# Kernel optimization log

Hardware: AMD Instinct MI355X
Metric: run time of the kernel (lower is better)

Reference implementation:

```python
import jax, jax.numpy as jnp
import numpy as np

B, Hres, Wres, DIM = 2, 56, 56, 256
HEADS, K = 8, 7


def setup_inputs() -> dict:
    key = jax.random.key(0)
    ks = jax.random.split(key, 6)
    return {
        "x": jax.random.normal(ks[0], (B, Hres, Wres, DIM), dtype=jnp.float32),
        "q_extra": jax.random.normal(ks[1], (B, Hres, Wres, DIM), dtype=jnp.float32),
        "kv_w": jax.random.normal(ks[2], (2 * DIM, DIM), dtype=jnp.float32) * 0.02,
        "kv_b": jnp.zeros((2 * DIM,), dtype=jnp.float32),
        "rpb": jax.random.normal(ks[3], (HEADS, 2 * K - 1, 2 * K - 1), dtype=jnp.float32) * 0.02,
        "proj_w": jax.random.normal(ks[4], (DIM, DIM), dtype=jnp.float32) * 0.02,
        "proj_b": jnp.zeros((DIM,), dtype=jnp.float32),
    }


def _window_idx(L, k):
    # NATTEN clamped window start: clip(i - k//2, 0, L - k)
    r = k // 2
    start = jnp.clip(jnp.arange(L) - r, 0, L - k)  # [L]
    return start[:, None] + jnp.arange(k)[None, :]  # [L, k]


def _pb_idx(L, k):
    # NATTEN relative-position-bias start index per query position
    r = k // 2
    i = jnp.arange(L)
    pb_start = r + jnp.maximum(r - i, 0) + jnp.minimum(L - i - 1 - r, 0)  # [L]
    return pb_start[:, None] + jnp.arange(k)[None, :]  # [L, k]


def reference(x, q_extra, kv_w, kv_b, rpb, proj_w, proj_b):
    Bn, H, W, C = x.shape
    heads = rpb.shape[0]
    k = (rpb.shape[1] + 1) // 2
    hd = C // heads
    scale = hd ** (-0.5)

    # q: [B, heads, H, W, hd]
    q = q_extra.reshape(Bn, H, W, heads, hd).transpose(0, 3, 1, 2, 4) * scale
    # kv projection -> key, value: [B, heads, H, W, hd]
    kv = (x @ kv_w.T + kv_b).reshape(Bn, H, W, 2, heads, hd).transpose(3, 0, 4, 1, 2, 5)
    key, val = kv[0], kv[1]

    idx_h = _window_idx(H, k)  # [H, k]
    idx_w = _window_idx(W, k)  # [W, k]

    # gather neighborhood windows: [B, heads, H, k, W, k, hd]
    k_win = key[:, :, idx_h][:, :, :, :, idx_w]
    v_win = val[:, :, idx_h][:, :, :, :, idx_w]

    # QK over neighborhood: [B, heads, H, W, k, k]
    attn = jnp.einsum('nhijd,nhiajbd->nhijab', q, k_win)

    # relative positional bias: [heads, H, k, W, k] -> [heads, H, W, k, k]
    pb_i = _pb_idx(H, k)
    pb_j = _pb_idx(W, k)
    bias = rpb[:, pb_i[:, :, None, None], pb_j[None, None, :, :]]
    attn = attn + bias.transpose(0, 1, 3, 2, 4)[None]

    attn = jax.nn.softmax(attn.reshape(Bn, heads, H, W, k * k), axis=-1)
    attn = attn.reshape(Bn, heads, H, W, k, k)

    # AV: [B, heads, H, W, hd]
    out = jnp.einsum('nhijab,nhiajbd->nhijd', attn, v_win)
    out = out.transpose(0, 2, 3, 1, 4).reshape(Bn, H, W, C)
    return out @ proj_w.T + proj_b
```

## Files before the change

kernel.cpp:

```cpp
#include <hip/hip_runtime.h>
#include <hip/hip_bf16.h>

#define BB 2
#define HH 56
#define WW 56
#define CC 256
#define HEADS 8
#define HD 32
#define KW 7
#define NPIX (BB*HH*WW)
#define KV_N 512

using bf16x8 = __attribute__((ext_vector_type(8))) short;
using f32x4  = __attribute__((ext_vector_type(4))) float;

__device__ __forceinline__ ushort f2bf(float f) {
    union { float f; uint u; } v; v.f = f;
    uint r = v.u + 0x7FFF + ((v.u >> 16) & 1);
    return (ushort)(r >> 16);
}
__device__ __forceinline__ float bf2f(ushort h) {
    union { uint u; float f; } v; v.u = ((uint)h) << 16;
    return v.f;
}

template<int BM, int BN, bool A_BF16, bool OUT_BF16>
__global__ __launch_bounds__(256) void gemm_bf16_nt(
    const void* __restrict__ Av, const float* __restrict__ Wt,
    const float* __restrict__ bias, void* __restrict__ Cv,
    int M, int N, int Kd)
{
    constexpr int BK  = 64;
    constexpr int LDT = 72;
    constexpr int WTM = BM / 2, WTN = BN / 2;
    constexpr int MF  = WTM / 16, NF = WTN / 16;

    __shared__ ushort As[BM][LDT];
    __shared__ ushort Bs[BN][LDT];

    const int tid  = threadIdx.x;
    const int lane = tid & 63;
    const int wid  = tid >> 6;
    const int wm   = wid >> 1;
    const int wn   = wid & 1;
    const int bm   = blockIdx.y * BM;
    const int bn   = blockIdx.x * BN;

    const int srow = tid >> 3;
    const int skq  = (tid & 7) * 8;

    f32x4 acc[MF][NF] = {};

    for (int k0 = 0; k0 < Kd; k0 += BK) {
        #pragma unroll
        for (int p = 0; p < BM / 32; ++p) {
            const int r = p * 32 + srow;
            if constexpr (A_BF16) {
                const ushort* src = (const ushort*)Av + (size_t)(bm + r) * Kd + k0 + skq;
                *(bf16x8*)&As[r][skq] = *(const bf16x8*)src;
            } else {
                const float* src = (const float*)Av + (size_t)(bm + r) * Kd + k0 + skq;
                float4 f0 = *(const float4*)(src);
                float4 f1 = *(const float4*)(src + 4);
                bf16x8 v;
                v[0]=f2bf(f0.x); v[1]=f2bf(f0.y); v[2]=f2bf(f0.z); v[3]=f2bf(f0.w);
                v[4]=f2bf(f1.x); v[5]=f2bf(f1.y); v[6]=f2bf(f1.z); v[7]=f2bf(f1.w);
                *(bf16x8*)&As[r][skq] = v;
            }
        }
        #pragma unroll
        for (int p = 0; p < BN / 32; ++p) {
            const int r = p * 32 + srow;
            const float* src = Wt + (size_t)(bn + r) * Kd + k0 + skq;
            float4 f0 = *(const float4*)(src);
            float4 f1 = *(const float4*)(src + 4);
            bf16x8 v;
            v[0]=f2bf(f0.x); v[1]=f2bf(f0.y); v[2]=f2bf(f0.z); v[3]=f2bf(f0.w);
            v[4]=f2bf(f1.x); v[5]=f2bf(f1.y); v[6]=f2bf(f1.z); v[7]=f2bf(f1.w);
            *(bf16x8*)&Bs[r][skq] = v;
        }
        __syncthreads();

        #pragma unroll
        for (int ks = 0; ks < 2; ++ks) {
            const int koff = ks * 32 + (lane >> 4) * 8;
            bf16x8 af[MF], bf[NF];
            #pragma unroll
            for (int m = 0; m < MF; ++m)
                af[m] = *(const bf16x8*)&As[wm*WTM + m*16 + (lane & 15)][koff];
            #pragma unroll
            for (int n = 0; n < NF; ++n)
                bf[n] = *(const bf16x8*)&Bs[wn*WTN + n*16 + (lane & 15)][koff];
            #pragma unroll
            for (int m = 0; m < MF; ++m)
                #pragma unroll
                for (int n = 0; n < NF; ++n)
                    acc[m][n] = __builtin_amdgcn_mfma_f32_16x16x32_bf16(af[m], bf[n], acc[m][n], 0, 0, 0);
        }
        __syncthreads();
    }

    #pragma unroll
    for (int n = 0; n < NF; ++n) {
        const int col = bn + wn*WTN + n*16 + (lane & 15);
        const float bval = bias[col];
        #pragma unroll
        for (int m = 0; m < MF; ++m) {
            const int row0 = bm + wm*WTM + m*16 + (lane >> 4) * 4;
            #pragma unroll
            for (int r = 0; r < 4; ++r) {
                const float o = acc[m][n][r] + bval;
                if constexpr (OUT_BF16)
                    ((ushort*)Cv)[(size_t)(row0 + r) * N + col] = f2bf(o);
                else
                    ((float*)Cv)[(size_t)(row0 + r) * N + col] = o;
            }
        }
    }
}

__global__ __launch_bounds__(256) void natt_tile(
    const float* __restrict__ q_extra, const ushort* __restrict__ kv,
    const float* __restrict__ rpb, ushort* __restrict__ attn_out)
{
    constexpr int LSTR = 40;
    __shared__ ushort Ks[196 * LSTR];
    __shared__ ushort Vs[196 * LSTR];

    const int blk  = blockIdx.x;
    const int head = blk & 7;
    const int t    = blk >> 3;
    const int tj   = t % 7;
    const int ti   = (t / 7) % 7;
    const int b    = t / 49;

    const int r0 = max(0, ti * 8 - 3);
    const int c0 = max(0, tj * 8 - 3);

    const int tid = threadIdx.x;

    for (int e = tid; e < 196 * 8; e += 256) {
        const int spix  = e >> 3;
        const int f4    = e & 7;
        const int half  = f4 >> 2;
        const int chunk = f4 & 3;
        const int wr   = spix / 14;
        const int wc   = spix - wr * 14;
        const int gr   = min(r0 + wr, HH - 1);
        const int gc   = min(c0 + wc, WW - 1);
        const ushort* src = kv + ((size_t)((b * HH + gr) * WW + gc)) * KV_N
                               + half * CC + head * HD + chunk * 8;
        ushort* dst = (half ? Vs : Ks) + spix * LSTR + chunk * 8;
        *(bf16x8*)dst = *(const bf16x8*)src;
    }

    const int sub = tid & 3;
    const int p   = tid >> 2;
    const int li  = p >> 3, lj = p & 7;
    const int i = ti * 8 + li, j = tj * 8 + lj;
    const int pix = (b * HH + i) * WW + j;
    const int d0 = sub * 8;

    const float scale = 0.17677669529663687f;
    float q[8];
    {
        const float* qp = q_extra + (size_t)pix * CC + head * HD + d0;
        float4 v0 = *(const float4*)(qp);
        float4 v1 = *(const float4*)(qp + 4);
        q[0]=v0.x*scale; q[1]=v0.y*scale; q[2]=v0.z*scale; q[3]=v0.w*scale;
        q[4]=v1.x*scale; q[5]=v1.y*scale; q[6]=v1.z*scale; q[7]=v1.w*scale;
    }

    const int sh = min(max(i - 3, 0), HH - KW);
    const int sw = min(max(j - 3, 0), WW - KW);
    const int wr0 = sh - r0;
    const int wc0 = sw - c0;
    const int pbi0 = sh - i + 6;
    const int pbj0 = sw - j + 6;

    __syncthreads();

    float s[49];
    float mmax = -3.4e38f;
    #pragma unroll
    for (int a = 0; a < KW; ++a) {
        const ushort* kr = &Ks[((wr0 + a) * 14 + wc0) * LSTR + d0];
        const float* bp = rpb + (size_t)head * 169 + (size_t)(pbi0 + a) * 13 + pbj0;
        #pragma unroll
        for (int c = 0; c < KW; ++c) {
            bf16x8 kk = *(const bf16x8*)(kr + c * LSTR);
            float v = q[0]*bf2f((ushort)kk[0]) + q[1]*bf2f((ushort)kk[1])
                    + q[2]*bf2f((ushort)kk[2]) + q[3]*bf2f((ushort)kk[3])
                    + q[4]*bf2f((ushort)kk[4]) + q[5]*bf2f((ushort)kk[5])
                    + q[6]*bf2f((ushort)kk[6]) + q[7]*bf2f((ushort)kk[7]);
            v += __shfl_xor(v, 1);
            v += __shfl_xor(v, 2);
            v += bp[c];
            s[a * KW + c] = v;
            mmax = fmaxf(mmax, v);
        }
    }

    float sum = 0.f;
    #pragma unroll
    for (int k = 0; k < KW * KW; ++k) {
        s[k] = __expf(s[k] - mmax);
        sum += s[k];
    }
    const float inv = 1.0f / sum;

    float acc[8] = {};
    #pragma unroll
    for (int a = 0; a < KW; ++a) {
        const ushort* vr = &Vs[((wr0 + a) * 14 + wc0) * LSTR + d0];
        #pragma unroll
        for (int c = 0; c < KW; ++c) {
            bf16x8 vv = *(const bf16x8*)(vr + c * LSTR);
            const float w = s[a * KW + c];
            acc[0] += w*bf2f((ushort)vv[0]); acc[1] += w*bf2f((ushort)vv[1]);
            acc[2] += w*bf2f((ushort)vv[2]); acc[3] += w*bf2f((ushort)vv[3]);
            acc[4] += w*bf2f((ushort)vv[4]); acc[5] += w*bf2f((ushort)vv[5]);
            acc[6] += w*bf2f((ushort)vv[6]); acc[7] += w*bf2f((ushort)vv[7]);
        }
    }

    ushort* op = attn_out + (size_t)pix * CC + head * HD + d0;
    bf16x8 o;
    o[0]=f2bf(acc[0]*inv); o[1]=f2bf(acc[1]*inv);
    o[2]=f2bf(acc[2]*inv); o[3]=f2bf(acc[3]*inv);
    o[4]=f2bf(acc[4]*inv); o[5]=f2bf(acc[5]*inv);
    o[6]=f2bf(acc[6]*inv); o[7]=f2bf(acc[7]*inv);
    *(bf16x8*)op = o;
}

extern "C" void kernel_launch(void* const* d_in, const int* in_sizes, int n_in,
                              void* d_out, int out_size, void* d_ws, size_t ws_size,
                              hipStream_t stream) {
    const float* x       = (const float*)d_in[0];
    const float* q_extra = (const float*)d_in[1];
    const float* kv_w    = (const float*)d_in[2];
    const float* kv_b    = (const float*)d_in[3];
    const float* rpb     = (const float*)d_in[4];
    const float* proj_w  = (const float*)d_in[5];
    const float* proj_b  = (const float*)d_in[6];
    float* out = (float*)d_out;

    ushort* kv       = (ushort*)d_ws;
    ushort* attn_out = kv + (size_t)NPIX * KV_N;

    {
        dim3 grid(KV_N/64, NPIX/64);
        gemm_bf16_nt<64,64,false,true><<<grid, 256, 0, stream>>>(x, kv_w, kv_b, kv, NPIX, KV_N, CC);
    }
    {
        dim3 grid(BB * 49 * HEADS);
        natt_tile<<<grid, 256, 0, stream>>>(q_extra, kv, rpb, attn_out);
    }
    {
        dim3 grid(CC/64, NPIX/64);
        gemm_bf16_nt<64,64,true,false><<<grid, 256, 0, stream>>>(attn_out, proj_w, proj_b, out, NPIX, CC, CC);
    }
}
```

Baseline: 118.9 us.

## Shrink attention tiles to 8x4, stage bias in LDS, use DPP reductions

Reshapes the neighborhood-attention tile from 8x8 to 8x4 query pixels per block, halving the block to 128 threads and doubling the grid so more blocks are available to spread across CUs. The K/V window shrinks to 14x10 pixels, which raises the halo overhead per output pixel. The relative-position bias table for the head is copied into shared memory instead of being read from global memory per score. The butterfly reductions now use DPP quad permutes instead of shuffles.

```diff
diff --git a/kernel.cpp b/kernel.cpp
--- a/kernel.cpp
+++ b/kernel.cpp
@@ -22,6 +22,13 @@
 __device__ __forceinline__ float bf2f(ushort h) {
     union { uint u; float f; } v; v.u = ((uint)h) << 16;
     return v.f;
+}
+template<int CTRL>
+__device__ __forceinline__ float dpp_qadd(float v) {
+    union { float f; int i; } a, b;
+    a.f = v;
+    b.i = __builtin_amdgcn_update_dpp(0, a.i, CTRL, 0xF, 0xF, true);
+    return v + b.f;
 }
 
 template<int BM, int BN, bool A_BF16, bool OUT_BF16>
@@ -119,33 +126,42 @@
     }
 }
 
-__global__ __launch_bounds__(256) void natt_tile(
+#define TI_H 8
+#define TJ_W 4
+#define WIN_R 14
+#define WIN_C 10
+#define NWPIX (WIN_R*WIN_C)
+#define LSTR 40
+__global__ __launch_bounds__(128) void natt_tile(
     const float* __restrict__ q_extra, const ushort* __restrict__ kv,
     const float* __restrict__ rpb, ushort* __restrict__ attn_out)
 {
-    constexpr int LSTR = 40;
-    __shared__ ushort Ks[196 * LSTR];
-    __shared__ ushort Vs[196 * LSTR];
+    __shared__ ushort Ks[NWPIX * LSTR];
+    __shared__ ushort Vs[NWPIX * LSTR];
+    __shared__ float  Bias[169];
 
     const int blk  = blockIdx.x;
     const int head = blk & 7;
     const int t    = blk >> 3;
-    const int tj   = t % 7;
-    const int ti   = (t / 7) % 7;
-    const int b    = t / 49;
-
-    const int r0 = max(0, ti * 8 - 3);
-    const int c0 = max(0, tj * 8 - 3);
+    const int tj   = t % 14;
+    const int ti   = (t / 14) % 7;
+    const int b    = t / 98;
+
+    const int r0 = max(0, ti * TI_H - 3);
+    const int c0 = max(0, tj * TJ_W - 3);
 
     const int tid = threadIdx.x;
 
-    for (int e = tid; e < 196 * 8; e += 256) {
+    for (int e = tid; e < 169; e += 128)
+        Bias[e] = rpb[head * 169 + e];
+
+    for (int e = tid; e < NWPIX * 8; e += 128) {
         const int spix  = e >> 3;
         const int f4    = e & 7;
         const int half  = f4 >> 2;
         const int chunk = f4 & 3;
-        const int wr   = spix / 14;
-        const int wc   = spix - wr * 14;
+        const int wr   = spix / WIN_C;
+        const int wc   = spix - wr * WIN_C;
         const int gr   = min(r0 + wr, HH - 1);
         const int gc   = min(c0 + wc, WW - 1);
         const ushort* src = kv + ((size_t)((b * HH + gr) * WW + gc)) * KV_N
@@ -156,8 +172,8 @@
 
     const int sub = tid & 3;
     const int p   = tid >> 2;
-    const int li  = p >> 3, lj = p & 7;
-    const int i = ti * 8 + li, j = tj * 8 + lj;
+    const int li  = p >> 2, lj = p & 3;
+    const int i = ti * TI_H + li, j = tj * TJ_W + lj;
     const int pix = (b * HH + i) * WW + j;
     const int d0 = sub * 8;
 
@@ -184,8 +200,8 @@
     float mmax = -3.4e38f;
     #pragma unroll
     for (int a = 0; a < KW; ++a) {
-        const ushort* kr = &Ks[((wr0 + a) * 14 + wc0) * LSTR + d0];
-        const float* bp = rpb + (size_t)head * 169 + (size_t)(pbi0 + a) * 13 + pbj0;
+        const ushort* kr = &Ks[((wr0 + a) * WIN_C + wc0) * LSTR + d0];
+        const float* bp = &Bias[(pbi0 + a) * 13 + pbj0];
         #pragma unroll
         for (int c = 0; c < KW; ++c) {
             bf16x8 kk = *(const bf16x8*)(kr + c * LSTR);
@@ -193,8 +209,8 @@
                     + q[2]*bf2f((ushort)kk[2]) + q[3]*bf2f((ushort)kk[3])
                     + q[4]*bf2f((ushort)kk[4]) + q[5]*bf2f((ushort)kk[5])
                     + q[6]*bf2f((ushort)kk[6]) + q[7]*bf2f((ushort)kk[7]);
-            v += __shfl_xor(v, 1);
-            v += __shfl_xor(v, 2);
+            v = dpp_qadd<0xB1>(v);
+            v = dpp_qadd<0x4E>(v);
             v += bp[c];
             s[a * KW + c] = v;
             mmax = fmaxf(mmax, v);
@@ -212,7 +228,7 @@
     float acc[8] = {};
     #pragma unroll
     for (int a = 0; a < KW; ++a) {
-        const ushort* vr = &Vs[((wr0 + a) * 14 + wc0) * LSTR + d0];
+        const ushort* vr = &Vs[((wr0 + a) * WIN_C + wc0) * LSTR + d0];
         #pragma unroll
         for (int c = 0; c < KW; ++c) {
             bf16x8 vv = *(const bf16x8*)(vr + c * LSTR);
@@ -253,8 +269,8 @@
         gemm_bf16_nt<64,64,false,true><<<grid, 256, 0, stream>>>(x, kv_w, kv_b, kv, NPIX, KV_N, CC);
     }
     {
-        dim3 grid(BB * 49 * HEADS);
-        natt_tile<<<grid, 256, 0, stream>>>(q_extra, kv, rpb, attn_out);
+        dim3 grid(BB * 7 * 14 * HEADS);
+        natt_tile<<<grid, 128, 0, stream>>>(q_extra, kv, rpb, attn_out);
     }
     {
         dim3 grid(CC/64, NPIX/64);
```

Result: faster. 114.0 us (-4.1%).
